# Kernel optimization log

Measured on AMD Instinct MI355X. Metric: run time of the kernel, lower is better.

Reference implementation:

```python
import jax, jax.numpy as jnp
import numpy as np

B, C, H, W = 16, 128, 64, 64
K, P = 16, 3  # number of basis functions, spline degree


def _open_uniform_knots(K, p):
    # [low x (p+1), interior, high x (p+1)], total K+p+1 knots on [-1, 1]
    n_interior = K - p - 1
    interior = np.linspace(-1.0, 1.0, n_interior + 2)[1:-1] if n_interior > 0 else np.zeros((0,))
    knots = np.concatenate([np.full(p + 1, -1.0), interior, np.full(p + 1, 1.0)])
    return jnp.asarray(knots, dtype=jnp.float32)


def _bspline_basis(x, knots, p):
    # Cox-de Boor recursion. x: (...,), knots: (K+p+1,) -> basis (..., K)
    Kn = knots.shape[0] - p - 1
    L = Kn + p
    xe = x[..., None]
    t0, t1 = knots[:-1], knots[1:]
    N = ((xe >= t0) & (xe < t1)).astype(x.dtype)
    # right-closed at the last knot: basis = e_{L-1}
    last_onehot = jnp.zeros((L,), x.dtype).at[L - 1].set(1.0)
    N = jnp.where(xe == knots[-1], last_onehot, N)
    for r in range(1, p + 1):
        Lr = Kn + p - (r - 1)
        left_den = knots[r:r + Lr - 1] - knots[:Lr - 1]
        right_den = knots[r + 1:r + Lr] - knots[1:Lr]
        safe_ld = jnp.where(left_den != 0, left_den, 1.0)
        safe_rd = jnp.where(right_den != 0, right_den, 1.0)
        left = jnp.where(left_den != 0, (xe - knots[:Lr - 1]) / safe_ld * N[..., :Lr - 1], 0.0)
        right = jnp.where(right_den != 0, (knots[r + 1:r + Lr] - xe) / safe_rd * N[..., 1:Lr], 0.0)
        N = left + right
    return N  # (..., K)


def setup_inputs() -> dict:
    key = jax.random.key(0)
    ks = jax.random.split(key, 6)
    x = jax.random.normal(ks[0], (B, C, H, W), dtype=jnp.float32)
    a = 1.0 + 0.1 * jax.random.normal(ks[1], (C,), dtype=jnp.float32)
    b = 0.1 * jax.random.normal(ks[2], (C,), dtype=jnp.float32)
    alpha = 0.1 * jax.random.normal(ks[3], (C, K), dtype=jnp.float32)
    id_gain = 1.0 + 0.1 * jax.random.normal(ks[4], (C,), dtype=jnp.float32)
    bias = 0.1 * jax.random.normal(ks[5], (C,), dtype=jnp.float32)
    return {"x": x, "a": a, "b": b, "alpha": alpha, "id_gain": id_gain, "bias": bias}


def reference(x, a, b, alpha, id_gain, bias):
    knots = _open_uniform_knots(K, P)
    ac = a[None, :, None, None]
    bc = b[None, :, None, None]
    x_aff = jnp.clip(x * ac + bc, -1.5, 1.5)
    basis = _bspline_basis(x_aff, knots, P)            # (B,C,H,W,K)
    spline_val = jnp.einsum('bchwk,ck->bchw', basis, alpha)
    return id_gain[None, :, None, None] * x + spline_val + bias[None, :, None, None]
```

## Files before the change

### kernel.cpp

```cpp
#include <hip/hip_runtime.h>


#define N_TOTAL (16 * 128 * 64 * 64)

__global__ __launch_bounds__(256) void kan_spline_kernel(
    const float* __restrict__ x,
    const float* __restrict__ a,
    const float* __restrict__ b,
    const float* __restrict__ alpha,
    const float* __restrict__ gain,
    const float* __restrict__ bias,
    float* __restrict__ out,
    int n4)
{
    int i = blockIdx.x * blockDim.x + threadIdx.x;
    if (i >= n4) return;

    const int c = (i >> 10) & 127;
    const float ac  = a[c];
    const float bc  = b[c];
    const float gc  = gain[c];
    const float bic = bias[c];
    const float* __restrict__ ar = alpha + (c << 4);

    const float h    = 2.0f / 13.0f;
    const float invh = 6.5f;

    float4 xv = reinterpret_cast<const float4*>(x)[i];
    float4 ov;

    auto knot = [&](int m) -> float {
        return fminf(fmaxf(fmaf((float)(m - 3), h, -1.0f), -1.0f), 1.0f);
    };
    auto invD3 = [&](int m) -> float {
        return (m == 1 || m == 15) ? invh
             : ((m == 2 || m == 14) ? 0.5f * invh : invh * (1.0f / 3.0f));
    };

#pragma unroll
    for (int e = 0; e < 4; ++e) {
        const float xs = (&xv.x)[e];
        float t = fminf(fmaxf(fmaf(xs, ac, bc), -1.5f), 1.5f);

        int s = (int)floorf((t + 1.0f) * invh);
        s = min(max(s, 0), 12);
        const int j = s + 3;

        const float left1  = t - knot(j);
        const float right1 = knot(j + 1) - t;
        const float left2  = t - knot(j - 1);
        const float right2 = knot(j + 2) - t;
        const float left3  = t - knot(j - 2);
        const float right3 = knot(j + 3) - t;

        const float invD2_jm1 = (j == 3)  ? invh : 0.5f * invh;
        const float invD2_j   = (j == 15) ? invh : 0.5f * invh;
        const float invD3_jm2 = invD3(j - 2);
        const float invD3_jm1 = invD3(j - 1);
        const float invD3_j   = invD3(j);

        float N0, N1, N2, N3, temp, saved;
        temp = invh;
        N0 = right1 * temp;
        N1 = left1 * temp;
        temp  = N0 * invD2_jm1;
        N0    = right1 * temp;
        saved = left2 * temp;
        temp  = N1 * invD2_j;
        N1    = saved + right2 * temp;
        N2    = left1 * temp;
        temp  = N0 * invD3_jm2;
        N0    = right1 * temp;
        saved = left3 * temp;
        temp  = N1 * invD3_jm1;
        N1    = saved + right2 * temp;
        saved = left2 * temp;
        temp  = N2 * invD3_j;
        N2    = saved + right3 * temp;
        N3    = left1 * temp;

        float spline = N0 * ar[s] + N1 * ar[s + 1] + N2 * ar[s + 2] + N3 * ar[s + 3];

        const bool inside = (t >= -1.0f) && (t < 1.0f);
        spline = inside ? spline : 0.0f;

        (&ov.x)[e] = fmaf(gc, xs, spline + bic);
    }

    reinterpret_cast<float4*>(out)[i] = ov;
}

extern "C" void kernel_launch(void* const* d_in, const int* in_sizes, int n_in,
                              void* d_out, int out_size, void* d_ws, size_t ws_size,
                              hipStream_t stream) {
    const float* x     = (const float*)d_in[0];
    const float* a     = (const float*)d_in[1];
    const float* b     = (const float*)d_in[2];
    const float* alpha = (const float*)d_in[3];
    const float* gain  = (const float*)d_in[4];
    const float* bias  = (const float*)d_in[5];
    float* out = (float*)d_out;

    const int n4 = out_size / 4;
    const int block = 256;
    const int grid = (n4 + block - 1) / block;
    kan_spline_kernel<<<grid, block, 0, stream>>>(x, a, b, alpha, gain, bias, out, n4);
}
```

Baseline: 95.68 us.

## Precompute per-span cubic polynomial coefficients and evaluate splines via Horner

Adds a small pre-kernel that converts each channel's B-spline weights into per-interval cubic polynomial coefficients, computed by sampling four points per span and taking finite differences. The main kernel then does a single float4 coefficient load and a Horner evaluation per element instead of running the Cox-de Boor recursion with four gathered alpha loads. This cuts ALU work in what is likely a memory-bound elementwise kernel. It costs an extra kernel launch, a workspace buffer, and possible small floating-point differences from the polynomial reconstruction.

```diff
diff --git a/kernel.cpp b/kernel.cpp
--- a/kernel.cpp
+++ b/kernel.cpp
@@ -1,15 +1,91 @@
 #include <hip/hip_runtime.h>
 
 
-#define N_TOTAL (16 * 128 * 64 * 64)
+__device__ __forceinline__ float knot_val(int m) {
+    const float h = 2.0f / 13.0f;
+    return fminf(fmaxf(fmaf((float)(m - 3), h, -1.0f), -1.0f), 1.0f);
+}
+
+__device__ __forceinline__ void basis_span(float t, int j,
+                                           float& N0, float& N1, float& N2, float& N3) {
+    const float invh = 6.5f;
+    auto invD3 = [&](int m) -> float {
+        return (m == 1 || m == 15) ? invh
+             : ((m == 2 || m == 14) ? 0.5f * invh : invh * (1.0f / 3.0f));
+    };
+    const float left1  = t - knot_val(j);
+    const float right1 = knot_val(j + 1) - t;
+    const float left2  = t - knot_val(j - 1);
+    const float right2 = knot_val(j + 2) - t;
+    const float left3  = t - knot_val(j - 2);
+    const float right3 = knot_val(j + 3) - t;
+    const float invD2_jm1 = (j == 3)  ? invh : 0.5f * invh;
+    const float invD2_j   = (j == 15) ? invh : 0.5f * invh;
+
+    float temp, saved;
+    temp = invh;
+    N0 = right1 * temp;
+    N1 = left1 * temp;
+    temp  = N0 * invD2_jm1;
+    N0    = right1 * temp;
+    saved = left2 * temp;
+    temp  = N1 * invD2_j;
+    N1    = saved + right2 * temp;
+    N2    = left1 * temp;
+    temp  = N0 * invD3(j - 2);
+    N0    = right1 * temp;
+    saved = left3 * temp;
+    temp  = N1 * invD3(j - 1);
+    N1    = saved + right2 * temp;
+    saved = left2 * temp;
+    temp  = N2 * invD3(j);
+    N2    = saved + right3 * temp;
+    N3    = left1 * temp;
+}
+
+__global__ __launch_bounds__(256) void kan_coeff_kernel(
+    const float* __restrict__ alpha,
+    float4* __restrict__ coef)
+{
+    int tid = blockIdx.x * blockDim.x + threadIdx.x;
+    if (tid >= 128 * 13) return;
+    const int c = tid / 13;
+    const int s = tid - c * 13;
+    const int j = s + 3;
+    const float h = 2.0f / 13.0f;
+
+    const float a0 = alpha[(c << 4) + s];
+    const float a1 = alpha[(c << 4) + s + 1];
+    const float a2 = alpha[(c << 4) + s + 2];
+    const float a3 = alpha[(c << 4) + s + 3];
+
+    float y[4];
+#pragma unroll
+    for (int k = 0; k < 4; ++k) {
+        const float u = (float)k * (1.0f / 3.0f);
+        const float t = fmaf((float)s + u, h, -1.0f);
+        float N0, N1, N2, N3;
+        basis_span(t, j, N0, N1, N2, N3);
+        y[k] = N0 * a0 + N1 * a1 + N2 * a2 + N3 * a3;
+    }
+    const float d1 = y[1] - y[0];
+    const float d2 = y[2] - 2.0f * y[1] + y[0];
+    const float d3 = y[3] - 3.0f * y[2] + 3.0f * y[1] - y[0];
+    float4 cf;
+    cf.x = y[0];
+    cf.y = 3.0f * d1 - 1.5f * d2 + d3;
+    cf.z = 4.5f * d2 - 4.5f * d3;
+    cf.w = 4.5f * d3;
+    coef[tid] = cf;
+}
 
 __global__ __launch_bounds__(256) void kan_spline_kernel(
     const float* __restrict__ x,
     const float* __restrict__ a,
     const float* __restrict__ b,
-    const float* __restrict__ alpha,
     const float* __restrict__ gain,
     const float* __restrict__ bias,
+    const float4* __restrict__ coef,
     float* __restrict__ out,
     int n4)
 {
@@ -21,70 +97,23 @@
     const float bc  = b[c];
     const float gc  = gain[c];
     const float bic = bias[c];
-    const float* __restrict__ ar = alpha + (c << 4);
-
-    const float h    = 2.0f / 13.0f;
-    const float invh = 6.5f;
+    const float4* __restrict__ Ct = coef + c * 13;
 
     float4 xv = reinterpret_cast<const float4*>(x)[i];
     float4 ov;
 
-    auto knot = [&](int m) -> float {
-        return fminf(fmaxf(fmaf((float)(m - 3), h, -1.0f), -1.0f), 1.0f);
-    };
-    auto invD3 = [&](int m) -> float {
-        return (m == 1 || m == 15) ? invh
-             : ((m == 2 || m == 14) ? 0.5f * invh : invh * (1.0f / 3.0f));
-    };
-
 #pragma unroll
     for (int e = 0; e < 4; ++e) {
         const float xs = (&xv.x)[e];
-        float t = fminf(fmaxf(fmaf(xs, ac, bc), -1.5f), 1.5f);
-
-        int s = (int)floorf((t + 1.0f) * invh);
+        const float t = fminf(fmaxf(fmaf(xs, ac, bc), -1.5f), 1.5f);
+        const float f = fmaf(t, 6.5f, 6.5f);
+        int s = (int)f;
         s = min(max(s, 0), 12);
-        const int j = s + 3;
-
-        const float left1  = t - knot(j);
-        const float right1 = knot(j + 1) - t;
-        const float left2  = t - knot(j - 1);
-        const float right2 = knot(j + 2) - t;
-        const float left3  = t - knot(j - 2);
-        const float right3 = knot(j + 3) - t;
-
-        const float invD2_jm1 = (j == 3)  ? invh : 0.5f * invh;
-        const float invD2_j   = (j == 15) ? invh : 0.5f * invh;
-        const float invD3_jm2 = invD3(j - 2);
-        const float invD3_jm1 = invD3(j - 1);
-        const float invD3_j   = invD3(j);
-
-        float N0, N1, N2, N3, temp, saved;
-        temp = invh;
-        N0 = right1 * temp;
-        N1 = left1 * temp;
-        temp  = N0 * invD2_jm1;
-        N0    = right1 * temp;
-        saved = left2 * temp;
-        temp  = N1 * invD2_j;
-        N1    = saved + right2 * temp;
-        N2    = left1 * temp;
-        temp  = N0 * invD3_jm2;
-        N0    = right1 * temp;
-        saved = left3 * temp;
-        temp  = N1 * invD3_jm1;
-        N1    = saved + right2 * temp;
-        saved = left2 * temp;
-        temp  = N2 * invD3_j;
-        N2    = saved + right3 * temp;
-        N3    = left1 * temp;
-
-        float spline = N0 * ar[s] + N1 * ar[s + 1] + N2 * ar[s + 2] + N3 * ar[s + 3];
-
-        const bool inside = (t >= -1.0f) && (t < 1.0f);
-        spline = inside ? spline : 0.0f;
-
-        (&ov.x)[e] = fmaf(gc, xs, spline + bic);
+        const float u = f - (float)s;
+        const float4 cf = Ct[s];
+        float p = fmaf(fmaf(fmaf(cf.w, u, cf.z), u, cf.y), u, cf.x);
+        p = (t >= -1.0f && t < 1.0f) ? p : 0.0f;
+        (&ov.x)[e] = fmaf(gc, xs, p + bic);
     }
 
     reinterpret_cast<float4*>(out)[i] = ov;
@@ -100,9 +129,12 @@
     const float* gain  = (const float*)d_in[4];
     const float* bias  = (const float*)d_in[5];
     float* out = (float*)d_out;
+    float4* coef = (float4*)d_ws;
+
+    kan_coeff_kernel<<<(128 * 13 + 255) / 256, 256, 0, stream>>>(alpha, coef);
 
     const int n4 = out_size / 4;
     const int block = 256;
     const int grid = (n4 + block - 1) / block;
-    kan_spline_kernel<<<grid, block, 0, stream>>>(x, a, b, alpha, gain, bias, out, n4);
+    kan_spline_kernel<<<grid, block, 0, stream>>>(x, a, b, gain, bias, coef, out, n4);
 }
```

Measured after the change: 95.36 us. No clear change (-0.3%).
